# Kernel optimization log

Measured on AMD Instinct MI355X. Metric: run time of the kernel, lower is better.

The kernel has to match this reference:

```python
import jax, jax.numpy as jnp
import numpy as np

B, S = 32, 2048
DIM_ACTION = 32
DIM_STRUCT = 64
HIDDEN = 128  # mlp_hidden_dim default = dim_action * 4
EPS = 1e-12   # F.normalize eps


def l2norm(t):
    n = jnp.linalg.norm(t, axis=-1, keepdims=True)
    return t / jnp.maximum(n, EPS)


def setup_inputs() -> dict:
    key = jax.random.key(0)
    ks = jax.random.split(key, 9)
    sd = lambda fan_in: 1.0 / np.sqrt(fan_in)
    inp = {
        "actions": jax.random.normal(ks[0], (B, S, DIM_ACTION), dtype=jnp.float32),
        # MLP: dim_action -> hidden -> hidden -> dim_structure^2 (depth=2 hidden relu layers)
        "w0": jax.random.uniform(ks[1], (DIM_ACTION, HIDDEN), jnp.float32, -sd(DIM_ACTION), sd(DIM_ACTION)),
        "b0": jnp.zeros((HIDDEN,), jnp.float32),
        "w1": jax.random.uniform(ks[2], (HIDDEN, HIDDEN), jnp.float32, -sd(HIDDEN), sd(HIDDEN)),
        "b1": jnp.zeros((HIDDEN,), jnp.float32),
        "w2": jax.random.uniform(ks[3], (HIDDEN, DIM_STRUCT * DIM_STRUCT), jnp.float32, -sd(HIDDEN), sd(HIDDEN)),
        "b2": jnp.zeros((DIM_STRUCT * DIM_STRUCT,), jnp.float32),
        # RNN init hidden parameter [1, dim_structure], ~N(0, 0.01)
        "init_hidden": jax.random.normal(ks[4], (1, DIM_STRUCT), dtype=jnp.float32) * 0.01,
    }
    return inp


def reference(actions, w0, b0, w1, b1, w2, b2, init_hidden):
    # MLP to transitions: [B, S, d*d]
    h = jax.nn.relu(jnp.einsum("bsa,ah->bsh", actions, w0) + b0)
    h = jax.nn.relu(jnp.einsum("bsh,hk->bsk", h, w1) + b1)
    t = jnp.einsum("bsh,ho->bso", h, w2) + b2
    transitions = t.reshape(B, S, DIM_STRUCT, DIM_STRUCT)  # [B, S, i, j]

    # RNN: hidden_{t+1} = l2norm(relu(hidden_t @ T_t)), scanned over seq
    hidden0 = jnp.broadcast_to(l2norm(init_hidden), (B, DIM_STRUCT))

    def step(hidden, trans):  # trans: [B, i, j]
        hidden = jnp.einsum("bi,bij->bj", hidden, trans)
        hidden = l2norm(jax.nn.relu(hidden))
        return hidden, hidden

    trans_seq = jnp.swapaxes(transitions, 0, 1)  # [S, B, i, j]
    _, hiddens = jax.lax.scan(step, hidden0, trans_seq)  # [S, B, d]
    return jnp.swapaxes(hiddens, 0, 1)  # [B, S, d]
```

## Files before the change

### kernel.cpp

```cpp
#include <hip/hip_runtime.h>

#define B_ 32
#define S_ 2048
#define DA 32
#define DH 128
#define DS 64
#define DS2 4096
#define TKK 16

template <int CTRL>
__device__ __forceinline__ float dpp_add(float x) {
  int t = __builtin_amdgcn_update_dpp(0, __float_as_int(x), CTRL, 0xF, 0xF, true);
  return x + __int_as_float(t);
}
__device__ __forceinline__ float row_sum16(float x) {
  x = dpp_add<0xB1>(x);
  x = dpp_add<0x4E>(x);
  x = dpp_add<0x141>(x);
  x = dpp_add<0x140>(x);
  return x;
}

__device__ __forceinline__ void gl2lds16(const float* g, float* l) {
  __builtin_amdgcn_global_load_lds(
      (const __attribute__((address_space(1))) void*)g,
      (__attribute__((address_space(3))) void*)l, 16, 0, 0);
}

struct SharedRnn {
  float4 ring[6][16][64];
  int flags[6];
  int cons;
};
struct SharedGemm {
  float As[2][TKK][128];
  float Bs[2][TKK][128];
};
struct SharedMlp {
  float a_t[DA][64];
  float w0_l[DA][DH];
  float h0t[DH][64];
};
union SharedU {
  SharedRnn r;
  SharedGemm g;
  SharedMlp m;
};

__device__ __forceinline__ void mlp_tile(
    const float* __restrict__ actions, const float* __restrict__ w0,
    const float* __restrict__ b0, const float* __restrict__ w1,
    const float* __restrict__ b1, float* __restrict__ h1t,
    int s_base, int M, int m0, SharedMlp& sm, int tid)
{
#pragma unroll
  for (int q = 0; q < 2; ++q) {
    int g = tid + 256 * q;
    int tok = g >> 3, kq = g & 7;
    int tl = m0 + tok;
    int b = tl & 31, s = s_base + (tl >> 5);
    float4 v = *(const float4*)(actions + ((size_t)b * S_ + s) * DA + 4 * kq);
    sm.a_t[4 * kq + 0][tok] = v.x; sm.a_t[4 * kq + 1][tok] = v.y;
    sm.a_t[4 * kq + 2][tok] = v.z; sm.a_t[4 * kq + 3][tok] = v.w;
  }
#pragma unroll
  for (int q = 0; q < 4; ++q) {
    int g = tid + 256 * q;
    ((float4*)&sm.w0_l[0][0])[g] = ((const float4*)w0)[g];
  }
  __syncthreads();

  const int tm = tid & 15;
  const int tn = tid >> 4;

  float acc[4][8];
#pragma unroll
  for (int mi = 0; mi < 4; ++mi)
#pragma unroll
    for (int ni = 0; ni < 8; ++ni) acc[mi][ni] = 0.f;

#pragma unroll 4
  for (int k = 0; k < DA; ++k) {
    float4 a4 = *(const float4*)&sm.a_t[k][4 * tm];
    float4 wa = *(const float4*)&sm.w0_l[k][8 * tn];
    float4 wb = *(const float4*)&sm.w0_l[k][8 * tn + 4];
    float av[4] = {a4.x, a4.y, a4.z, a4.w};
    float wv[8] = {wa.x, wa.y, wa.z, wa.w, wb.x, wb.y, wb.z, wb.w};
#pragma unroll
    for (int mi = 0; mi < 4; ++mi)
#pragma unroll
      for (int ni = 0; ni < 8; ++ni) acc[mi][ni] += av[mi] * wv[ni];
  }
  {
    float4 ba = *(const float4*)(b0 + 8 * tn);
    float4 bb = *(const float4*)(b0 + 8 * tn + 4);
    float bv[8] = {ba.x, ba.y, ba.z, ba.w, bb.x, bb.y, bb.z, bb.w};
#pragma unroll
    for (int mi = 0; mi < 4; ++mi)
#pragma unroll
      for (int ni = 0; ni < 8; ++ni)
        sm.h0t[8 * tn + ni][4 * tm + mi] = fmaxf(acc[mi][ni] + bv[ni], 0.f);
  }
  __syncthreads();

  float acc1[4][8];
#pragma unroll
  for (int mi = 0; mi < 4; ++mi)
#pragma unroll
    for (int ni = 0; ni < 8; ++ni) acc1[mi][ni] = 0.f;

#pragma unroll 4
  for (int k = 0; k < DH; ++k) {
    float4 h4 = *(const float4*)&sm.h0t[k][4 * tm];
    float4 wa = *(const float4*)(w1 + (size_t)k * DH + 8 * tn);
    float4 wb = *(const float4*)(w1 + (size_t)k * DH + 8 * tn + 4);
    float av[4] = {h4.x, h4.y, h4.z, h4.w};
    float wv[8] = {wa.x, wa.y, wa.z, wa.w, wb.x, wb.y, wb.z, wb.w};
#pragma unroll
    for (int mi = 0; mi < 4; ++mi)
#pragma unroll
      for (int ni = 0; ni < 8; ++ni) acc1[mi][ni] += av[mi] * wv[ni];
  }
  {
    float4 ba = *(const float4*)(b1 + 8 * tn);
    float4 bb = *(const float4*)(b1 + 8 * tn + 4);
    float bv[8] = {ba.x, ba.y, ba.z, ba.w, bb.x, bb.y, bb.z, bb.w};
#pragma unroll
    for (int ni = 0; ni < 8; ++ni) {
      float4 o;
      o.x = fmaxf(acc1[0][ni] + bv[ni], 0.f);
      o.y = fmaxf(acc1[1][ni] + bv[ni], 0.f);
      o.z = fmaxf(acc1[2][ni] + bv[ni], 0.f);
      o.w = fmaxf(acc1[3][ni] + bv[ni], 0.f);
      *(float4*)(h1t + (size_t)(8 * tn + ni) * M + m0 + 4 * tm) = o;
    }
  }
}

__device__ __forceinline__ void trans_tile(
    const float* __restrict__ h1t, const float* __restrict__ w2,
    const float* __restrict__ b2, float* __restrict__ trans,
    int M, int n0, int m0, SharedGemm& sg, int tid)
{
  const int w  = tid >> 6;
  const int lw = tid & 63;

  auto aload = [&](int t, int buf) {
#pragma unroll
    for (int ii = 0; ii < 2; ++ii) {
      const int i = 2 * w + ii;
      const int kr = 2 * i + (lw >> 5);
      const int c4 = 4 * (lw & 31);
      gl2lds16(h1t + (size_t)(t * TKK + kr) * M + m0 + c4, &sg.As[buf][2 * i][0]);
      gl2lds16(w2 + (size_t)(t * TKK + kr) * DS2 + n0 + c4, &sg.Bs[buf][2 * i][0]);
    }
  };

  aload(0, 0);

  const int mg = tid >> 4;
  const int ng = tid & 15;
  float acc[8][8];
#pragma unroll
  for (int mi = 0; mi < 8; ++mi)
#pragma unroll
    for (int ni = 0; ni < 8; ++ni) acc[mi][ni] = 0.f;

  int buf = 0;
  for (int t = 0; t < DH / TKK; ++t) {
    __syncthreads();
    if (t < DH / TKK - 1) aload(t + 1, buf ^ 1);
#pragma unroll
    for (int k = 0; k < TKK; ++k) {
      float4 a0 = *(const float4*)&sg.As[buf][k][8 * mg];
      float4 a1 = *(const float4*)&sg.As[buf][k][8 * mg + 4];
      float av[8] = {a0.x, a0.y, a0.z, a0.w, a1.x, a1.y, a1.z, a1.w};
      float4 b0v = *(const float4*)&sg.Bs[buf][k][4 * ng];
      float4 b1v = *(const float4*)&sg.Bs[buf][k][64 + 4 * ng];
      float bv[8] = {b0v.x, b0v.y, b0v.z, b0v.w, b1v.x, b1v.y, b1v.z, b1v.w};
#pragma unroll
      for (int mi = 0; mi < 8; ++mi)
#pragma unroll
        for (int ni = 0; ni < 8; ++ni) acc[mi][ni] += av[mi] * bv[ni];
    }
    buf ^= 1;
  }

  float4 bb0 = *(const float4*)(b2 + n0 + 4 * ng);
  float4 bb1 = *(const float4*)(b2 + n0 + 64 + 4 * ng);
  float bv[8] = {bb0.x, bb0.y, bb0.z, bb0.w, bb1.x, bb1.y, bb1.z, bb1.w};
#pragma unroll
  for (int mi = 0; mi < 8; ++mi) {
    float* dst = trans + (size_t)(m0 + 8 * mg + mi) * DS2 + n0;
#pragma unroll
    for (int q = 0; q < 2; ++q) {
      float4 o;
      o.x = acc[mi][4 * q + 0] + bv[4 * q + 0];
      o.y = acc[mi][4 * q + 1] + bv[4 * q + 1];
      o.z = acc[mi][4 * q + 2] + bv[4 * q + 2];
      o.w = acc[mi][4 * q + 3] + bv[4 * q + 3];
      *(float4*)(dst + 64 * q + 4 * ng) = o;
    }
  }
}

__global__ __launch_bounds__(256) void k_mlp01(
    const float* __restrict__ actions, const float* __restrict__ w0,
    const float* __restrict__ b0, const float* __restrict__ w1,
    const float* __restrict__ b1, float* __restrict__ h1t,
    int s_base, int M)
{
  __shared__ SharedMlp sm;
  mlp_tile(actions, w0, b0, w1, b1, h1t, s_base, M, blockIdx.x * 64, sm,
           threadIdx.x);
}

__global__ __launch_bounds__(256, 1) void k_comb(
    const float* __restrict__ actions, const float* __restrict__ w0,
    const float* __restrict__ b0, const float* __restrict__ w1,
    const float* __restrict__ b1, const float* __restrict__ w2,
    const float* __restrict__ b2, const float* __restrict__ init_hidden,
    float* __restrict__ trans0, float* __restrict__ trans1,
    float* __restrict__ h1t0, float* __restrict__ h1t1,
    float* __restrict__ hstate, float* __restrict__ out,
    int c, int SC, int nch)
{
  __shared__ SharedU sh;
  const int tid = threadIdx.x;
  const int M = SC * 32;

  if (blockIdx.x >= 32) {
    const int bi = blockIdx.x - 32;
    if (c < nch) {
      const float* h1t = (c & 1) ? h1t1 : h1t0;
      float* trans = (c & 1) ? trans1 : trans0;
      const int NJ = (M / 128) * (DS2 / 128);
      for (int j = bi; j < NJ; j += 224) {
        const int mt = j >> 5, nt = j & 31;
        trans_tile(h1t, w2, b2, trans, M, nt * 128, mt * 128, sh.g, tid);
        __syncthreads();
      }
      if (c + 1 < nch) {
        __syncthreads();
        float* h1n = ((c + 1) & 1) ? h1t1 : h1t0;
        for (int j = bi; j < M / 64; j += 224) {
          mlp_tile(actions, w0, b0, w1, b1, h1n, (c + 1) * SC, M, j * 64,
                   sh.m, tid);
          __syncthreads();
        }
      }
    }
    return;
  }

  if (c == 0) return;
  const int cc = c - 1;
  const float* trans = (cc & 1) ? trans1 : trans0;
  const int s_base = cc * SC;
  const int wv = tid >> 6;
  const int lane = tid & 63;
  const int b = blockIdx.x;

  if (tid < 6) sh.r.flags[tid] = 0;
  if (tid == 6) sh.r.cons = 0;
  __syncthreads();

  const float* base = trans + (size_t)b * DS2;

  if (wv > 0) {
    const int p = wv - 1;
    int prev = -1;
    for (int s = p; s < SC; s += 3) {
      while (s - __hip_atomic_load(&sh.r.cons, __ATOMIC_RELAXED,
                                   __HIP_MEMORY_SCOPE_WORKGROUP) > 5)
        __builtin_amdgcn_s_sleep(2);
      const int slot = s % 6;
      const float* g = base + (size_t)s * (32 * DS2) + 4 * lane;
      float* l = (float*)&sh.r.ring[slot][0][0];
#pragma unroll
      for (int q = 0; q < 16; ++q)
        gl2lds16(g + q * 256, l + q * 256);
      if (prev >= 0) {
        asm volatile("s_waitcnt vmcnt(16)" ::: "memory");
        __hip_atomic_store(&sh.r.flags[prev % 6], prev + 1, __ATOMIC_RELAXED,
                           __HIP_MEMORY_SCOPE_WORKGROUP);
      }
      prev = s;
    }
    if (prev >= 0) {
      asm volatile("s_waitcnt vmcnt(0)" ::: "memory");
      __hip_atomic_store(&sh.r.flags[prev % 6], prev + 1, __ATOMIC_RELAXED,
                         __HIP_MEMORY_SCOPE_WORKGROUP);
    }
  } else {
    const int d = lane >> 4;
    const int cq = lane & 15;
    const bool d1 = (d & 1), d2 = (d & 2);
    const int pb = lane & 48;

    float4 hq;
    if (cc == 0) {
      hq = *(const float4*)(init_hidden + 4 * cq);
      float ss0 = row_sum16(hq.x * hq.x + hq.y * hq.y + hq.z * hq.z + hq.w * hq.w);
      float iv0 = 1.0f / fmaxf(sqrtf(ss0), 1e-12f);
      hq.x *= iv0; hq.y *= iv0; hq.z *= iv0; hq.w *= iv0;
    } else {
      hq = *(const float4*)(hstate + b * DS + 4 * cq);
    }
    float inv_prev = 1.0f;

    float* outp = out + ((size_t)b * S_ + s_base) * DS + 4 * cq;
    int fpre = -1;
    for (int s = 0; s < SC; ++s) {
      const int slot = s % 6;
      if (fpre < s + 1) {
        while (__hip_atomic_load(&sh.r.flags[slot], __ATOMIC_ACQUIRE,
                                 __HIP_MEMORY_SCOPE_WORKGROUP) < s + 1)
          __builtin_amdgcn_s_sleep(0);
      }
      fpre = __hip_atomic_load(&sh.r.flags[(s + 1) % 6], __ATOMIC_ACQUIRE,
                               __HIP_MEMORY_SCOPE_WORKGROUP);

      float hsel = d2 ? (d1 ? hq.w : hq.z) : (d1 ? hq.y : hq.x);
      float ax = 0.f, ay = 0.f, az = 0.f, aw = 0.f;
#pragma unroll
      for (int q = 0; q < 16; ++q) {
        float4 t4 = sh.r.ring[slot][q][lane];
        float hb = __shfl(hsel, pb + q, 64);
        ax += hb * t4.x; ay += hb * t4.y;
        az += hb * t4.z; aw += hb * t4.w;
      }
      __hip_atomic_store(&sh.r.cons, s + 1, __ATOMIC_RELAXED,
                         __HIP_MEMORY_SCOPE_WORKGROUP);

      ax += __shfl_xor(ax, 16, 64); ax += __shfl_xor(ax, 32, 64);
      ay += __shfl_xor(ay, 16, 64); ay += __shfl_xor(ay, 32, 64);
      az += __shfl_xor(az, 16, 64); az += __shfl_xor(az, 32, 64);
      aw += __shfl_xor(aw, 16, 64); aw += __shfl_xor(aw, 32, 64);
      hq.x = fmaxf(ax * inv_prev, 0.f);
      hq.y = fmaxf(ay * inv_prev, 0.f);
      hq.z = fmaxf(az * inv_prev, 0.f);
      hq.w = fmaxf(aw * inv_prev, 0.f);
      float ss = row_sum16(hq.x * hq.x + hq.y * hq.y + hq.z * hq.z + hq.w * hq.w);
      float inv = 1.0f / fmaxf(sqrtf(ss), 1e-12f);
      if (d == 0) {
        float4 o;
        o.x = hq.x * inv; o.y = hq.y * inv; o.z = hq.z * inv; o.w = hq.w * inv;
        *(float4*)(outp + (size_t)s * DS) = o;
      }
      inv_prev = inv;
    }
    if (d == 0) {
      float4 o;
      o.x = hq.x * inv_prev; o.y = hq.y * inv_prev;
      o.z = hq.z * inv_prev; o.w = hq.w * inv_prev;
      *(float4*)(hstate + b * DS + 4 * cq) = o;
    }
  }
}

extern "C" void kernel_launch(void* const* d_in, const int* in_sizes, int n_in,
                              void* d_out, int out_size, void* d_ws, size_t ws_size,
                              hipStream_t stream) {
  const float* actions     = (const float*)d_in[0];
  const float* w0          = (const float*)d_in[1];
  const float* b0          = (const float*)d_in[2];
  const float* w1          = (const float*)d_in[3];
  const float* b1          = (const float*)d_in[4];
  const float* w2          = (const float*)d_in[5];
  const float* b2          = (const float*)d_in[6];
  const float* init_hidden = (const float*)d_in[7];
  float* out = (float*)d_out;

  int SC = 2048;
  while (SC > 4) {
    size_t need = 2 * ((size_t)SC * 32 * DS2 * 4 + (size_t)SC * 32 * DH * 4)
                + (size_t)B_ * DS * 4;
    if (need <= ws_size) break;
    SC >>= 1;
  }
  float* trans0 = (float*)d_ws;
  float* trans1 = trans0 + (size_t)SC * 32 * DS2;
  float* h1t0   = trans1 + (size_t)SC * 32 * DS2;
  float* h1t1   = h1t0 + (size_t)SC * 32 * DH;
  float* hstate = h1t1 + (size_t)SC * 32 * DH;

  const int M = SC * 32;
  const int nch = S_ / SC;

  hipLaunchKernelGGL(k_mlp01, dim3(M / 64), dim3(256), 0, stream,
                     actions, w0, b0, w1, b1, h1t0, 0, M);
  for (int c = 0; c <= nch; ++c) {
    hipLaunchKernelGGL(k_comb, dim3(256), dim3(256), 0, stream,
                       actions, w0, b0, w1, b1, w2, b2, init_hidden,
                       trans0, trans1, h1t0, h1t1, hstate, out, c, SC, nch);
  }
}
```

Measured before the change: 1.630 ms.

## Replace LDS ring producer-consumer RNN with single-wave register double-buffered prefetch

The RNN phase used to run three producer waves that streamed transition matrices into an LDS ring with flag-based handshakes to one consumer wave. Now only one wave runs per batch. It loads each step's 64x64 matrix straight into registers, double-buffered two steps ahead, so LDS round trips and the atomic flag polling leave the serial recurrence. The cost is 128 extra VGPRs of buffering and a prefetch depth of only two steps, which may not hide global memory latency as well as the six-deep ring. A padding member keeps the shared union at its original size.

```diff
diff --git a/kernel.cpp b/kernel.cpp
--- a/kernel.cpp
+++ b/kernel.cpp
@@ -27,11 +27,6 @@
       (__attribute__((address_space(3))) void*)l, 16, 0, 0);
 }
 
-struct SharedRnn {
-  float4 ring[6][16][64];
-  int flags[6];
-  int cons;
-};
 struct SharedGemm {
   float As[2][TKK][128];
   float Bs[2][TKK][128];
@@ -42,9 +37,9 @@
   float h0t[DH][64];
 };
 union SharedU {
-  SharedRnn r;
   SharedGemm g;
   SharedMlp m;
+  char pad[84 * 1024];
 };
 
 __device__ __forceinline__ void mlp_tile(
@@ -254,109 +249,87 @@
   }
 
   if (c == 0) return;
+  if (tid >= 64) return;
+  const int lane = tid;
+  const int b = blockIdx.x;
   const int cc = c - 1;
   const float* trans = (cc & 1) ? trans1 : trans0;
   const int s_base = cc * SC;
-  const int wv = tid >> 6;
-  const int lane = tid & 63;
-  const int b = blockIdx.x;
-
-  if (tid < 6) sh.r.flags[tid] = 0;
-  if (tid == 6) sh.r.cons = 0;
-  __syncthreads();
-
-  const float* base = trans + (size_t)b * DS2;
-
-  if (wv > 0) {
-    const int p = wv - 1;
-    int prev = -1;
-    for (int s = p; s < SC; s += 3) {
-      while (s - __hip_atomic_load(&sh.r.cons, __ATOMIC_RELAXED,
-                                   __HIP_MEMORY_SCOPE_WORKGROUP) > 5)
-        __builtin_amdgcn_s_sleep(2);
-      const int slot = s % 6;
-      const float* g = base + (size_t)s * (32 * DS2) + 4 * lane;
-      float* l = (float*)&sh.r.ring[slot][0][0];
-#pragma unroll
-      for (int q = 0; q < 16; ++q)
-        gl2lds16(g + q * 256, l + q * 256);
-      if (prev >= 0) {
-        asm volatile("s_waitcnt vmcnt(16)" ::: "memory");
-        __hip_atomic_store(&sh.r.flags[prev % 6], prev + 1, __ATOMIC_RELAXED,
-                           __HIP_MEMORY_SCOPE_WORKGROUP);
-      }
-      prev = s;
-    }
-    if (prev >= 0) {
-      asm volatile("s_waitcnt vmcnt(0)" ::: "memory");
-      __hip_atomic_store(&sh.r.flags[prev % 6], prev + 1, __ATOMIC_RELAXED,
-                         __HIP_MEMORY_SCOPE_WORKGROUP);
-    }
+
+  const int d = lane >> 4;
+  const int cq = lane & 15;
+  const bool d1 = (d & 1), d2 = (d & 2);
+  const int pb = lane & 48;
+
+  float4 hq;
+  if (cc == 0) {
+    hq = *(const float4*)(init_hidden + 4 * cq);
+    float ss0 = row_sum16(hq.x * hq.x + hq.y * hq.y + hq.z * hq.z + hq.w * hq.w);
+    float iv0 = 1.0f / fmaxf(sqrtf(ss0), 1e-12f);
+    hq.x *= iv0; hq.y *= iv0; hq.z *= iv0; hq.w *= iv0;
   } else {
-    const int d = lane >> 4;
-    const int cq = lane & 15;
-    const bool d1 = (d & 1), d2 = (d & 2);
-    const int pb = lane & 48;
-
-    float4 hq;
-    if (cc == 0) {
-      hq = *(const float4*)(init_hidden + 4 * cq);
-      float ss0 = row_sum16(hq.x * hq.x + hq.y * hq.y + hq.z * hq.z + hq.w * hq.w);
-      float iv0 = 1.0f / fmaxf(sqrtf(ss0), 1e-12f);
-      hq.x *= iv0; hq.y *= iv0; hq.z *= iv0; hq.w *= iv0;
-    } else {
-      hq = *(const float4*)(hstate + b * DS + 4 * cq);
-    }
-    float inv_prev = 1.0f;
-
-    float* outp = out + ((size_t)b * S_ + s_base) * DS + 4 * cq;
-    int fpre = -1;
-    for (int s = 0; s < SC; ++s) {
-      const int slot = s % 6;
-      if (fpre < s + 1) {
-        while (__hip_atomic_load(&sh.r.flags[slot], __ATOMIC_ACQUIRE,
-                                 __HIP_MEMORY_SCOPE_WORKGROUP) < s + 1)
-          __builtin_amdgcn_s_sleep(0);
-      }
-      fpre = __hip_atomic_load(&sh.r.flags[(s + 1) % 6], __ATOMIC_ACQUIRE,
-                               __HIP_MEMORY_SCOPE_WORKGROUP);
-
-      float hsel = d2 ? (d1 ? hq.w : hq.z) : (d1 ? hq.y : hq.x);
-      float ax = 0.f, ay = 0.f, az = 0.f, aw = 0.f;
-#pragma unroll
-      for (int q = 0; q < 16; ++q) {
-        float4 t4 = sh.r.ring[slot][q][lane];
-        float hb = __shfl(hsel, pb + q, 64);
-        ax += hb * t4.x; ay += hb * t4.y;
-        az += hb * t4.z; aw += hb * t4.w;
-      }
-      __hip_atomic_store(&sh.r.cons, s + 1, __ATOMIC_RELAXED,
-                         __HIP_MEMORY_SCOPE_WORKGROUP);
-
-      ax += __shfl_xor(ax, 16, 64); ax += __shfl_xor(ax, 32, 64);
-      ay += __shfl_xor(ay, 16, 64); ay += __shfl_xor(ay, 32, 64);
-      az += __shfl_xor(az, 16, 64); az += __shfl_xor(az, 32, 64);
-      aw += __shfl_xor(aw, 16, 64); aw += __shfl_xor(aw, 32, 64);
-      hq.x = fmaxf(ax * inv_prev, 0.f);
-      hq.y = fmaxf(ay * inv_prev, 0.f);
-      hq.z = fmaxf(az * inv_prev, 0.f);
-      hq.w = fmaxf(aw * inv_prev, 0.f);
-      float ss = row_sum16(hq.x * hq.x + hq.y * hq.y + hq.z * hq.z + hq.w * hq.w);
-      float inv = 1.0f / fmaxf(sqrtf(ss), 1e-12f);
-      if (d == 0) {
-        float4 o;
-        o.x = hq.x * inv; o.y = hq.y * inv; o.z = hq.z * inv; o.w = hq.w * inv;
-        *(float4*)(outp + (size_t)s * DS) = o;
-      }
-      inv_prev = inv;
-    }
-    if (d == 0) {
-      float4 o;
-      o.x = hq.x * inv_prev; o.y = hq.y * inv_prev;
-      o.z = hq.z * inv_prev; o.w = hq.w * inv_prev;
-      *(float4*)(hstate + b * DS + 4 * cq) = o;
-    }
-  }
+    hq = *(const float4*)(hstate + b * DS + 4 * cq);
+  }
+  float inv_prev = 1.0f;
+
+  const float* tb = trans + (size_t)b * DS2 + 4 * lane;
+  float4 sl0[16], sl1[16];
+
+#define PRELOAD(SLOT, sidx)                                                   \
+  {                                                                           \
+    const float* _p = tb + (size_t)(sidx) * (32 * DS2);                       \
+    _Pragma("unroll")                                                         \
+    for (int q = 0; q < 16; ++q) SLOT[q] = *(const float4*)(_p + q * 256);    \
+  }
+
+  PRELOAD(sl0, 0)
+  PRELOAD(sl1, 1)
+
+  float* outp = out + ((size_t)b * S_ + s_base) * DS + 4 * cq;
+
+#define RSTEP(SLOT, scur)                                                     \
+  {                                                                           \
+    float hsel = d2 ? (d1 ? hq.w : hq.z) : (d1 ? hq.y : hq.x);                \
+    float ax = 0.f, ay = 0.f, az = 0.f, aw = 0.f;                             \
+    _Pragma("unroll")                                                         \
+    for (int q = 0; q < 16; ++q) {                                            \
+      float hb = __shfl(hsel, pb + q, 64);                      \
+      ax += hb * SLOT[q].x; ay += hb * SLOT[q].y;                             \
+      az += hb * SLOT[q].z; aw += hb * SLOT[q].w;                             \
+    }                                                                         \
+    int sp = (scur) + 2; if (sp > SC - 1) sp = SC - 1;                        \
+    PRELOAD(SLOT, sp)                                                         \
+    ax += __shfl_xor(ax, 16, 64); ax += __shfl_xor(ax, 32, 64);               \
+    ay += __shfl_xor(ay, 16, 64); ay += __shfl_xor(ay, 32, 64);               \
+    az += __shfl_xor(az, 16, 64); az += __shfl_xor(az, 32, 64);               \
+    aw += __shfl_xor(aw, 16, 64); aw += __shfl_xor(aw, 32, 64);               \
+    hq.x = fmaxf(ax * inv_prev, 0.f);                                         \
+    hq.y = fmaxf(ay * inv_prev, 0.f);                                         \
+    hq.z = fmaxf(az * inv_prev, 0.f);                                         \
+    hq.w = fmaxf(aw * inv_prev, 0.f);                                         \
+    float ss = row_sum16(hq.x * hq.x + hq.y * hq.y + hq.z * hq.z + hq.w * hq.w); \
+    float inv = 1.0f / fmaxf(sqrtf(ss), 1e-12f);                              \
+    if (d == 0) {                                                             \
+      float4 o;                                                               \
+      o.x = hq.x * inv; o.y = hq.y * inv; o.z = hq.z * inv; o.w = hq.w * inv; \
+      *(float4*)(outp + (size_t)(scur) * DS) = o;                             \
+    }                                                                         \
+    inv_prev = inv;                                                           \
+  }
+
+  for (int s0 = 0; s0 < SC; s0 += 2) {
+    RSTEP(sl0, s0)
+    RSTEP(sl1, s0 + 1)
+  }
+
+  if (d == 0) {
+    float4 o;
+    o.x = hq.x * inv_prev; o.y = hq.y * inv_prev;
+    o.z = hq.z * inv_prev; o.w = hq.w * inv_prev;
+    *(float4*)(hstate + b * DS + 4 * cq) = o;
+  }
+#undef PRELOAD
+#undef RSTEP
 }
 
 extern "C" void kernel_launch(void* const* d_in, const int* in_sizes, int n_in,
```

After: 2.080 ms. 1.28x slower.

## Replace producer-wave ring with single-wave self-prefetching LDS pipeline in RNN

Applied to the files above, without the earlier changes.

The recurrence blocks no longer split work between three producer waves and one consumer wave that coordinate through LDS flags and spin loops. A single wave now streams transition matrices into a 4-slot LDS ring with direct global-to-LDS loads, keeping three steps in flight and gating each step with an `s_waitcnt vmcnt` count instead of atomics. The shared-memory union is padded to 84KB, which appears intended to limit how many blocks share a CU. The risk is lower memory-level parallelism from one issuing wave, and the conservative wait count also covers the interleaved output stores.

```diff
diff --git a/kernel.cpp b/kernel.cpp
--- a/kernel.cpp
+++ b/kernel.cpp
@@ -28,9 +28,7 @@
 }
 
 struct SharedRnn {
-  float4 ring[6][16][64];
-  int flags[6];
-  int cons;
+  float4 ring[4][16][64];
 };
 struct SharedGemm {
   float As[2][TKK][128];
@@ -45,6 +43,7 @@
   SharedRnn r;
   SharedGemm g;
   SharedMlp m;
+  char pad[84 * 1024];
 };
 
 __device__ __forceinline__ void mlp_tile(
@@ -254,108 +253,83 @@
   }
 
   if (c == 0) return;
+  if (tid >= 64) return;
+  const int lane = tid;
+  const int b = blockIdx.x;
   const int cc = c - 1;
   const float* trans = (cc & 1) ? trans1 : trans0;
   const int s_base = cc * SC;
-  const int wv = tid >> 6;
-  const int lane = tid & 63;
-  const int b = blockIdx.x;
-
-  if (tid < 6) sh.r.flags[tid] = 0;
-  if (tid == 6) sh.r.cons = 0;
-  __syncthreads();
-
-  const float* base = trans + (size_t)b * DS2;
-
-  if (wv > 0) {
-    const int p = wv - 1;
-    int prev = -1;
-    for (int s = p; s < SC; s += 3) {
-      while (s - __hip_atomic_load(&sh.r.cons, __ATOMIC_RELAXED,
-                                   __HIP_MEMORY_SCOPE_WORKGROUP) > 5)
-        __builtin_amdgcn_s_sleep(2);
-      const int slot = s % 6;
-      const float* g = base + (size_t)s * (32 * DS2) + 4 * lane;
-      float* l = (float*)&sh.r.ring[slot][0][0];
-#pragma unroll
-      for (int q = 0; q < 16; ++q)
-        gl2lds16(g + q * 256, l + q * 256);
-      if (prev >= 0) {
-        asm volatile("s_waitcnt vmcnt(16)" ::: "memory");
-        __hip_atomic_store(&sh.r.flags[prev % 6], prev + 1, __ATOMIC_RELAXED,
-                           __HIP_MEMORY_SCOPE_WORKGROUP);
-      }
-      prev = s;
-    }
-    if (prev >= 0) {
-      asm volatile("s_waitcnt vmcnt(0)" ::: "memory");
-      __hip_atomic_store(&sh.r.flags[prev % 6], prev + 1, __ATOMIC_RELAXED,
-                         __HIP_MEMORY_SCOPE_WORKGROUP);
-    }
+
+  const int d = lane >> 4;
+  const int cq = lane & 15;
+  const bool d1 = (d & 1), d2 = (d & 2);
+  const int pb = lane & 48;
+
+  float4 hq;
+  if (cc == 0) {
+    hq = *(const float4*)(init_hidden + 4 * cq);
+    float ss0 = row_sum16(hq.x * hq.x + hq.y * hq.y + hq.z * hq.z + hq.w * hq.w);
+    float iv0 = 1.0f / fmaxf(sqrtf(ss0), 1e-12f);
+    hq.x *= iv0; hq.y *= iv0; hq.z *= iv0; hq.w *= iv0;
   } else {
-    const int d = lane >> 4;
-    const int cq = lane & 15;
-    const bool d1 = (d & 1), d2 = (d & 2);
-    const int pb = lane & 48;
-
-    float4 hq;
-    if (cc == 0) {
-      hq = *(const float4*)(init_hidden + 4 * cq);
-      float ss0 = row_sum16(hq.x * hq.x + hq.y * hq.y + hq.z * hq.z + hq.w * hq.w);
-      float iv0 = 1.0f / fmaxf(sqrtf(ss0), 1e-12f);
-      hq.x *= iv0; hq.y *= iv0; hq.z *= iv0; hq.w *= iv0;
-    } else {
-      hq = *(const float4*)(hstate + b * DS + 4 * cq);
-    }
-    float inv_prev = 1.0f;
-
-    float* outp = out + ((size_t)b * S_ + s_base) * DS + 4 * cq;
-    int fpre = -1;
-    for (int s = 0; s < SC; ++s) {
-      const int slot = s % 6;
-      if (fpre < s + 1) {
-        while (__hip_atomic_load(&sh.r.flags[slot], __ATOMIC_ACQUIRE,
-                                 __HIP_MEMORY_SCOPE_WORKGROUP) < s + 1)
-          __builtin_amdgcn_s_sleep(0);
-      }
-      fpre = __hip_atomic_load(&sh.r.flags[(s + 1) % 6], __ATOMIC_ACQUIRE,
-                               __HIP_MEMORY_SCOPE_WORKGROUP);
-
-      float hsel = d2 ? (d1 ? hq.w : hq.z) : (d1 ? hq.y : hq.x);
-      float ax = 0.f, ay = 0.f, az = 0.f, aw = 0.f;
-#pragma unroll
-      for (int q = 0; q < 16; ++q) {
-        float4 t4 = sh.r.ring[slot][q][lane];
-        float hb = __shfl(hsel, pb + q, 64);
-        ax += hb * t4.x; ay += hb * t4.y;
-        az += hb * t4.z; aw += hb * t4.w;
-      }
-      __hip_atomic_store(&sh.r.cons, s + 1, __ATOMIC_RELAXED,
-                         __HIP_MEMORY_SCOPE_WORKGROUP);
-
-      ax += __shfl_xor(ax, 16, 64); ax += __shfl_xor(ax, 32, 64);
-      ay += __shfl_xor(ay, 16, 64); ay += __shfl_xor(ay, 32, 64);
-      az += __shfl_xor(az, 16, 64); az += __shfl_xor(az, 32, 64);
-      aw += __shfl_xor(aw, 16, 64); aw += __shfl_xor(aw, 32, 64);
-      hq.x = fmaxf(ax * inv_prev, 0.f);
-      hq.y = fmaxf(ay * inv_prev, 0.f);
-      hq.z = fmaxf(az * inv_prev, 0.f);
-      hq.w = fmaxf(aw * inv_prev, 0.f);
-      float ss = row_sum16(hq.x * hq.x + hq.y * hq.y + hq.z * hq.z + hq.w * hq.w);
-      float inv = 1.0f / fmaxf(sqrtf(ss), 1e-12f);
-      if (d == 0) {
-        float4 o;
-        o.x = hq.x * inv; o.y = hq.y * inv; o.z = hq.z * inv; o.w = hq.w * inv;
-        *(float4*)(outp + (size_t)s * DS) = o;
-      }
-      inv_prev = inv;
-    }
+    hq = *(const float4*)(hstate + b * DS + 4 * cq);
+  }
+  float inv_prev = 1.0f;
+
+  const float* tb0 = trans + (size_t)b * DS2;
+
+  auto dma = [&](int s) {
+    const float* g = tb0 + (size_t)s * (32 * DS2) + 4 * lane;
+    float* l = (float*)&sh.r.ring[s & 3][0][0];
+#pragma unroll
+    for (int q = 0; q < 16; ++q)
+      gl2lds16(g + q * 256, l + q * 256);
+  };
+
+  dma(0); dma(1); dma(2);
+
+  float* outp = out + ((size_t)b * S_ + s_base) * DS + 4 * cq;
+
+  for (int s = 0; s < SC; ++s) {
+    asm volatile("s_waitcnt vmcnt(32)" ::: "memory");
+    const int slot = s & 3;
+
+    float hsel = d2 ? (d1 ? hq.w : hq.z) : (d1 ? hq.y : hq.x);
+    float ax = 0.f, ay = 0.f, az = 0.f, aw = 0.f;
+#pragma unroll
+    for (int q = 0; q < 16; ++q) {
+      float4 t4 = sh.r.ring[slot][q][lane];
+      float hb = __shfl(hsel, pb + q, 64);
+      ax += hb * t4.x; ay += hb * t4.y;
+      az += hb * t4.z; aw += hb * t4.w;
+    }
+
+    int sp = s + 3; if (sp > SC - 1) sp = SC - 1;
+    dma(sp);
+
+    ax += __shfl_xor(ax, 16, 64); ax += __shfl_xor(ax, 32, 64);
+    ay += __shfl_xor(ay, 16, 64); ay += __shfl_xor(ay, 32, 64);
+    az += __shfl_xor(az, 16, 64); az += __shfl_xor(az, 32, 64);
+    aw += __shfl_xor(aw, 16, 64); aw += __shfl_xor(aw, 32, 64);
+    hq.x = fmaxf(ax * inv_prev, 0.f);
+    hq.y = fmaxf(ay * inv_prev, 0.f);
+    hq.z = fmaxf(az * inv_prev, 0.f);
+    hq.w = fmaxf(aw * inv_prev, 0.f);
+    float ss = row_sum16(hq.x * hq.x + hq.y * hq.y + hq.z * hq.z + hq.w * hq.w);
+    float inv = 1.0f / fmaxf(sqrtf(ss), 1e-12f);
     if (d == 0) {
       float4 o;
-      o.x = hq.x * inv_prev; o.y = hq.y * inv_prev;
-      o.z = hq.z * inv_prev; o.w = hq.w * inv_prev;
-      *(float4*)(hstate + b * DS + 4 * cq) = o;
-    }
+      o.x = hq.x * inv; o.y = hq.y * inv; o.z = hq.z * inv; o.w = hq.w * inv;
+      *(float4*)(outp + (size_t)s * DS) = o;
+    }
+    inv_prev = inv;
+  }
+
+  if (d == 0) {
+    float4 o;
+    o.x = hq.x * inv_prev; o.y = hq.y * inv_prev;
+    o.z = hq.z * inv_prev; o.w = hq.w * inv_prev;
+    *(float4*)(hstate + b * DS + 4 * cq) = o;
   }
 }
 
```

Result: slower. 1.999 ms (+22.6%).
